# Performance work log

Hardware: AMD Instinct MI355X
Metric: run time of the kernel (lower is better)

The kernel has to match this reference:

```python
import jax, jax.numpy as jnp
import numpy as np

V = 50257  # vocab_size
H = 512    # d_model
S = 512    # source length
B = 8      # batch
T = 64     # decode steps


def setup_inputs() -> dict:
    key = jax.random.key(0)
    k1, k2, k3, k4, k5, k6 = jax.random.split(key, 6)
    src_full = jax.random.randint(k1, (S, B), 0, V, dtype=jnp.int32)
    decode_output = jax.random.normal(k2, (T, B, H), dtype=jnp.float32)
    decode_attn = jax.random.uniform(k3, (B, T, S), dtype=jnp.float32)
    memory = jax.random.normal(k4, (S, B, H), dtype=jnp.float32)
    # learned params: gen_proj (H->V) and prob_proj (H->1)
    W_gen = jax.random.normal(k5, (H, V), dtype=jnp.float32) / np.sqrt(H)
    b_gen = jnp.zeros((V,), dtype=jnp.float32)
    W_prob = jax.random.normal(k6, (H, 1), dtype=jnp.float32) / np.sqrt(H)
    b_prob = jnp.zeros((1,), dtype=jnp.float32)
    return {
        "src_full": src_full,
        "decode_output": decode_output,
        "decode_attn": decode_attn,
        "memory": memory,
        "W_gen": W_gen,
        "b_gen": b_gen,
        "W_prob": W_prob,
        "b_prob": b_prob,
    }


def reference(src_full, decode_output, decode_attn, memory, W_gen, b_gen, W_prob, b_prob):
    # context[t,b,h] = sum_s attn[b,t,s] * memory[s,b,h]
    context = jnp.einsum("bts,sbh->tbh", decode_attn, memory)  # [T,B,H]
    prob = jax.nn.sigmoid(context @ W_prob + b_prob)           # [T,B,1] copy gate p_gen
    gen_logits = prob * jax.nn.softmax(decode_output @ W_gen + b_gen, axis=-1)  # [T,B,V]

    # scatter-add attention mass onto vocab slots: copy[t,b, src_full[s,b]] += attn[b,t,s]
    attn_tbs = jnp.transpose(decode_attn, (1, 0, 2))  # [T,B,S]
    idx = src_full.T                                  # [B,S]
    ti = jnp.arange(T)[:, None, None]
    bi = jnp.arange(B)[None, :, None]
    copy_logits = jnp.zeros((T, B, V), dtype=decode_attn.dtype).at[ti, bi, idx[None, :, :]].add(attn_tbs)
    copy_logits = (1.0 - prob) * jax.nn.softmax(copy_logits, axis=-1)

    return jnp.log(gen_logits + copy_logits)
```

## Files before the change

kernel.cpp:

```cpp
#include <hip/hip_runtime.h>
#include <hip/hip_bf16.h>
#include <math.h>

#define VV 50257
#define VP 50304
#define HH 512
#define SS 512
#define BB 8
#define TT 64
#define MM (TT*BB)

typedef __bf16 bf16x2 __attribute__((ext_vector_type(2)));
typedef __bf16 bf16x4 __attribute__((ext_vector_type(4)));
typedef __bf16 bf16x8 __attribute__((ext_vector_type(8)));
typedef float  f32x4  __attribute__((ext_vector_type(4)));

__device__ __forceinline__ __bf16 f2b(float f) {
    unsigned u = __builtin_bit_cast(unsigned, f);
    unsigned r = (u + 0x7fffu + ((u >> 16) & 1u)) >> 16;
    unsigned short s = (unsigned short)r;
    return __builtin_bit_cast(__bf16, s);
}

__device__ __forceinline__ void gl2lds16(const void* g, void* l) {
    __builtin_amdgcn_global_load_lds(
        (const __attribute__((address_space(1))) unsigned*)g,
        (__attribute__((address_space(3))) unsigned*)l, 16, 0, 0);
}

#define WAITV(n) asm volatile("s_waitcnt vmcnt(" #n ")" ::: "memory")

__global__ __launch_bounds__(256) void k_pre0(const float* __restrict__ A,
                                              __bf16* __restrict__ Ab,
                                              const float* __restrict__ mem,
                                              const float* __restrict__ Wp,
                                              float* __restrict__ mw) {
    int tid = threadIdx.x;
    if (blockIdx.x < 256) {
        int i = (blockIdx.x * 256 + tid) * 4;
        float4 v = *(const float4*)&A[i];
        bf16x4 o = {f2b(v.x), f2b(v.y), f2b(v.z), f2b(v.w)};
        *(bf16x4*)&Ab[i] = o;
    } else {
        int bx = blockIdx.x - 256;
        int row = bx * 4 + (tid >> 6);
        int lane = tid & 63;
        const float* mp = mem + (size_t)row * HH;
        float acc = 0.f;
#pragma unroll
        for (int i = 0; i < HH / 64; i++)
            acc += mp[lane + 64 * i] * Wp[lane + 64 * i];
#pragma unroll
        for (int off = 32; off > 0; off >>= 1) acc += __shfl_down(acc, off);
        if (lane == 0) mw[row] = acc;
    }
}

#define NWT (VP / 32)
__global__ __launch_bounds__(256) void k_wt2(const float* __restrict__ W,
                                             __bf16* __restrict__ Wt,
                                             const float* __restrict__ attn,
                                             const float* __restrict__ mw,
                                             const float* __restrict__ bp,
                                             float* __restrict__ prob,
                                             float* __restrict__ Z) {
    __shared__ float tile[2][32][33];
    __shared__ __bf16 Wo[32][520];
    int tid = threadIdx.x;

    if (blockIdx.x < NWT) {
        int n0 = blockIdx.x * 32;
        int nn = tid >> 3, ks = (tid & 7) * 4;
#pragma unroll
        for (int kc = 0; kc < 16; kc++) {
            int k0 = kc * 32;
            int p = kc & 1;
#pragma unroll
            for (int rd = 0; rd < 4; rd++) {
                int idx = rd * 256 + tid;
                int kk = idx >> 5, nc = idx & 31;
                int n = n0 + nc;
                tile[p][kk][nc] = (n < VV) ? W[(size_t)(k0 + kk) * VV + n] : 0.f;
            }
            __syncthreads();
            bf16x4 o = {f2b(tile[p][ks][nn]), f2b(tile[p][ks + 1][nn]),
                        f2b(tile[p][ks + 2][nn]), f2b(tile[p][ks + 3][nn])};
            *(bf16x4*)&Wo[nn][k0 + ks] = o;
        }
        __syncthreads();
#pragma unroll
        for (int i = 0; i < 8; i++) {
            int r = i * 4 + (tid >> 6);
            int c = (tid & 63) * 8;
            *(bf16x8*)&Wt[(size_t)(n0 + r) * HH + c] = *(const bf16x8*)&Wo[r][c];
        }
    } else {
        int r = blockIdx.x - NWT;
        int t = r / BB, b = r % BB;
        const float* ap = attn + ((size_t)b * TT + t) * SS;
        float acc = ap[tid] * mw[tid * BB + b] +
                    ap[tid + 256] * mw[(tid + 256) * BB + b];
        float* red = &tile[0][0][0];
        red[tid] = acc; __syncthreads();
        for (int st = 128; st > 0; st >>= 1) {
            if (tid < st) red[tid] += red[tid + st];
            __syncthreads();
        }
        if (tid == 0) {
            prob[r] = 1.f / (1.f + expf(-(red[0] + bp[0])));
            Z[r] = 0.f;
        }
    }
}

template<bool BF16OUT>
__global__ __launch_bounds__(512, 4) void k_gemm6(const __bf16* __restrict__ Ab,
                                                  const __bf16* __restrict__ Wt,
                                                  const float* __restrict__ bias,
                                                  float* __restrict__ Cf,
                                                  __bf16* __restrict__ Cb,
                                                  float* __restrict__ Zrow) {
    __shared__ __bf16 As[3][8192];
    __shared__ __bf16 Bs[3][4096];
    __shared__ float zred[256];

    const int tid  = threadIdx.x;
    const int lane = tid & 63;
    const int wave = tid >> 6;
    const int l15  = lane & 15;
    const int quad = lane >> 4;
    const int wr = (wave >> 1) * 64;
    const int wc = (wave & 1) * 64;

    int L = blockIdx.x + gridDim.x * blockIdx.y;
    int xcd = L & 7, i8 = L >> 3;
    int nid = (xcd < 2 ? xcd * 99 : 2 * 99 + (xcd - 2) * 98) + i8;
    const int row0 = (nid & 1) * 256;
    const int col0 = (nid >> 1) * 128;

    size_t offA[2];
#pragma unroll
    for (int q = 0; q < 2; q++)
        offA[q] = (size_t)(row0 + (2 * wave + q) * 16 + l15) * HH + quad * 8;
    const size_t offB = (size_t)(col0 + wave * 16 + l15) * HH + quad * 8;

#define STAGE(buf, k0)                                                       \
    do {                                                                     \
        gl2lds16(Ab + offA[0] + (k0), &As[buf][(2 * wave) * 512]);           \
        gl2lds16(Ab + offA[1] + (k0), &As[buf][(2 * wave + 1) * 512]);       \
        gl2lds16(Wt + offB + (k0),    &Bs[buf][wave * 512]);                 \
    } while (0)

    f32x4 acc[4][4] = {};

    STAGE(0, 0);
    STAGE(1, 32);
#pragma unroll
    for (int it = 0; it < 16; ++it) {
        if (it < 15) WAITV(3);
        else         WAITV(0);
        __builtin_amdgcn_s_barrier();
        if (it < 14) STAGE((it + 2) % 3, (it + 2) * 32);
        const __bf16* Al = &As[it % 3][0];
        const __bf16* Bl = &Bs[it % 3][0];
        bf16x8 af[4], bfv[4];
#pragma unroll
        for (int mt = 0; mt < 4; mt++)
            af[mt] = *(const bf16x8*)&Al[((wr >> 4) + mt) * 512 + lane * 8];
#pragma unroll
        for (int nt = 0; nt < 4; nt++)
            bfv[nt] = *(const bf16x8*)&Bl[((wc >> 4) + nt) * 512 + lane * 8];
        __builtin_amdgcn_s_setprio(1);
#pragma unroll
        for (int mt = 0; mt < 4; mt++)
#pragma unroll
            for (int nt = 0; nt < 4; nt++)
                acc[mt][nt] = __builtin_amdgcn_mfma_f32_16x16x32_bf16(
                    af[mt], bfv[nt], acc[mt][nt], 0, 0, 0);
        __builtin_amdgcn_s_setprio(0);
    }
#undef STAGE

    __syncthreads();
    if (tid < 256) zred[tid] = 0.f;
    __syncthreads();

#pragma unroll
    for (int mt = 0; mt < 4; mt++) {
        float esum[4] = {0.f, 0.f, 0.f, 0.f};
#pragma unroll
        for (int nt = 0; nt < 4; nt++) {
            int c = col0 + wc + nt * 16 + l15;
            if (c < VV) {
                float bv = bias[c];
#pragma unroll
                for (int i = 0; i < 4; i++) {
                    int r = row0 + wr + mt * 16 + quad * 4 + i;
                    float l = acc[mt][nt][i] + bv;
                    if (BF16OUT) Cb[(size_t)r * VP + c] = f2b(l);
                    else         Cf[(size_t)r * VV + c] = l;
                    esum[i] += __expf(l);
                }
            }
        }
#pragma unroll
        for (int i = 0; i < 4; i++) {
            float e = esum[i];
            e += __shfl_xor(e, 1);
            e += __shfl_xor(e, 2);
            e += __shfl_xor(e, 4);
            e += __shfl_xor(e, 8);
            if (l15 == 0)
                atomicAdd(&zred[wr + mt * 16 + quad * 4 + i], e);
        }
    }
    __syncthreads();
    if (tid < 256) atomicAdd(&Zrow[row0 + tid], zred[tid]);
}

#define HT 1024
#define NBW 1572

__device__ __forceinline__ void build_hash(const int* __restrict__ src,
                                           const float* __restrict__ ap,
                                           int b, int tid,
                                           int* keys, float* vals, unsigned* bmap,
                                           float* red, int* s_D, float* s_Zc) {
    for (int i = tid; i < HT; i += 256) { keys[i] = -1; vals[i] = 0.f; }
    for (int i = tid; i < NBW; i += 256) bmap[i] = 0u;
    if (tid == 0) *s_D = 0;
    __syncthreads();

    for (int s = tid; s < SS; s += 256) {
        int idx = src[s * BB + b];
        float v = ap[s];
        unsigned h = ((unsigned)idx * 2654435761u) >> 22;
        while (true) {
            int old = atomicCAS(&keys[h], -1, idx);
            if (old == -1 || old == idx) { atomicAdd(&vals[h], v); break; }
            h = (h + 1) & (HT - 1);
        }
    }
    __syncthreads();

    float lsum = 0.f; int dloc = 0;
    for (int i = tid; i < HT; i += 256) {
        int k = keys[i];
        if (k != -1) {
            lsum += __expf(vals[i]); dloc++;
            atomicOr(&bmap[(unsigned)k >> 5], 1u << (k & 31));
        }
    }
    atomicAdd(s_D, dloc);
    red[tid] = lsum; __syncthreads();
    for (int st = 128; st > 0; st >>= 1) {
        if (tid < st) red[tid] += red[tid + st];
        __syncthreads();
    }
    if (tid == 0) *s_Zc = (float)(VV - *s_D) + red[0];
    __syncthreads();
}

#define HV (VP / 2)
__global__ __launch_bounds__(1024) void k_final2(const int* __restrict__ src,
                                                 const float* __restrict__ attn,
                                                 const float* __restrict__ prob,
                                                 const float* __restrict__ Zrow,
                                                 const __bf16* __restrict__ LG,
                                                 float* __restrict__ out) {
    __shared__ int      keys[HT];
    __shared__ float    vals[HT];
    __shared__ unsigned bmap[NBW];
    __shared__ float    red[1024];
    __shared__ int      s_D;
    __shared__ float    s_Zc;

    int r = blockIdx.y;
    int half = blockIdx.x;
    int t = r / BB, b = r % BB;
    int tid = threadIdx.x;
    const float* ap = attn + ((size_t)b * TT + t) * SS;

    { keys[tid] = -1; vals[tid] = 0.f; }
    for (int i = tid; i < NBW; i += 1024) bmap[i] = 0u;
    if (tid == 0) s_D = 0;
    __syncthreads();

    if (tid < SS) {
        int idx = src[tid * BB + b];
        float v = ap[tid];
        unsigned h = ((unsigned)idx * 2654435761u) >> 22;
        while (true) {
            int old = atomicCAS(&keys[h], -1, idx);
            if (old == -1 || old == idx) { atomicAdd(&vals[h], v); break; }
            h = (h + 1) & (HT - 1);
        }
    }
    __syncthreads();

    float lsum = 0.f;
    {
        int k = keys[tid];
        bool occ = (k != -1);
        if (occ) {
            lsum = __expf(vals[tid]);
            atomicOr(&bmap[(unsigned)k >> 5], 1u << (k & 31));
        }
        unsigned long long m = __ballot(occ);
        if ((tid & 63) == 0) atomicAdd(&s_D, __popcll(m));
    }
    red[tid] = lsum; __syncthreads();
    for (int st = 512; st > 0; st >>= 1) {
        if (tid < st) red[tid] += red[tid + st];
        __syncthreads();
    }
    if (tid == 0) s_Zc = (float)(VV - s_D) + red[0];
    __syncthreads();

    float p = prob[r];
    float pinvZ = p / Zrow[r];
    float qinvZc = (1.f - p) / s_Zc;

    const __bf16* lrow = LG + (size_t)r * VP;
    float* orow = out + (size_t)r * VV;

    int base = half * HV;
    for (int v0 = base + tid * 8; v0 < base + HV; v0 += 8192) {
        bf16x8 l8 = *(const bf16x8*)&lrow[v0];
        unsigned bits = (bmap[v0 >> 5] >> (v0 & 31)) & 0xFFu;
        if (bits == 0u && v0 + 8 <= VV) {
#pragma unroll
            for (int e = 0; e < 8; e++)
                orow[v0 + e] = __logf(pinvZ * __expf((float)l8[e]) + qinvZc);
        } else {
#pragma unroll
            for (int e = 0; e < 8; e++) {
                int v = v0 + e;
                if (v < VV) {
                    float l = (float)l8[e];
                    float c = 1.f;
                    if ((bits >> e) & 1u) {
                        unsigned h = ((unsigned)v * 2654435761u) >> 22;
                        while (true) {
                            int k = keys[h];
                            if (k == v) { c = __expf(vals[h]); break; }
                            if (k == -1) break;
                            h = (h + 1) & (HT - 1);
                        }
                    }
                    orow[v] = __logf(pinvZ * __expf(l) + qinvZc * c);
                }
            }
        }
    }
}

#define CHUNKS 6283
__global__ __launch_bounds__(256) void k_final_s(const int* __restrict__ src,
                                                 const float* __restrict__ attn,
                                                 const float* __restrict__ prob,
                                                 const float* __restrict__ Zrow,
                                                 float* __restrict__ out) {
    __shared__ int      keys[HT];
    __shared__ float    vals[HT];
    __shared__ unsigned bmap[NBW];
    __shared__ float    red[256];
    __shared__ int      s_D;
    __shared__ float    s_Zc;

    int r = blockIdx.y;
    int t = r / BB, b = r % BB;
    int tid = threadIdx.x;
    const float* ap = attn + ((size_t)b * TT + t) * SS;
    build_hash(src, ap, b, tid, keys, vals, bmap, red, &s_D, &s_Zc);

    float p = prob[r];
    float pinvZ = p / Zrow[r];
    float qinvZc = (1.f - p) / s_Zc;

    int c0 = blockIdx.x * CHUNKS;
    int c1 = c0 + CHUNKS; if (c1 > VV) c1 = VV;
    float* rowp = out + (size_t)r * VV;

    for (int v = c0 + tid; v < c1; v += 256) {
        float l = rowp[v];
        float c = 1.f;
        if ((bmap[v >> 5] >> (v & 31)) & 1u) {
            unsigned h = ((unsigned)v * 2654435761u) >> 22;
            while (true) {
                int k = keys[h];
                if (k == v) { c = __expf(vals[h]); break; }
                if (k == -1) break;
                h = (h + 1) & (HT - 1);
            }
        }
        rowp[v] = __logf(pinvZ * __expf(l) + qinvZc * c);
    }
}

extern "C" void kernel_launch(void* const* d_in, const int* in_sizes, int n_in,
                              void* d_out, int out_size, void* d_ws, size_t ws_size,
                              hipStream_t stream) {
    const int*   src_full      = (const int*)d_in[0];
    const float* decode_output = (const float*)d_in[1];
    const float* decode_attn   = (const float*)d_in[2];
    const float* memory        = (const float*)d_in[3];
    const float* W_gen         = (const float*)d_in[4];
    const float* b_gen         = (const float*)d_in[5];
    const float* W_prob        = (const float*)d_in[6];
    const float* b_prob        = (const float*)d_in[7];
    float* out = (float*)d_out;

    float* ws   = (float*)d_ws;
    float* mw   = ws;
    float* prob = ws + 4096;
    float* Z    = ws + 4608;
    __bf16* Ab  = (__bf16*)(ws + 5120);
    __bf16* Wt  = (__bf16*)(ws + 5120 + 131072);
    __bf16* LG  = Wt + (size_t)VP * HH;

    size_t base_b = (size_t)(5120 + 131072) * sizeof(float);
    size_t wt_b   = (size_t)VP * HH * 2;
    size_t lg_b   = (size_t)MM * VP * 2;
    bool full = ws_size >= base_b + wt_b + lg_b;

    k_pre0<<<1280, 256, 0, stream>>>(decode_output, Ab, memory, W_prob, mw);
    k_wt2<<<NWT + 512, 256, 0, stream>>>(W_gen, Wt, decode_attn, mw, b_prob,
                                         prob, Z);

    dim3 ggrid(MM / 256, VP / 128);
    if (full) {
        k_gemm6<true><<<ggrid, 512, 0, stream>>>(Ab, Wt, b_gen, nullptr, LG, Z);
        dim3 fgrid(2, MM);
        k_final2<<<fgrid, 1024, 0, stream>>>(src_full, decode_attn, prob, Z, LG, out);
    } else {
        k_gemm6<false><<<ggrid, 512, 0, stream>>>(Ab, Wt, b_gen, out, nullptr, Z);
        dim3 fgrid((VV + CHUNKS - 1) / CHUNKS, MM);
        k_final_s<<<fgrid, 256, 0, stream>>>(src_full, decode_attn, prob, Z, out);
    }
}
```

Before: 359.0 us.

## Use k-blocked W layout to drop LDS transpose and fold gate into final kernel

Replaces the LDS-tiled transpose of W_gen with a direct conversion into a k-blocked layout (8 consecutive k values per vocab column), written with vectorized loads and bf16x8 stores. The GEMM B-operand addressing is changed to read this layout. The conversion is merged into the pre-processing kernel, which removes one launch and the shared-memory round trip. The sigmoid copy gate is now computed inside the final kernels via an extra reduction, and Z is zeroed with a memset. The cost is redundant gate computation per final block and possibly less cache-friendly B loads in the GEMM.

```diff
diff --git a/kernel.cpp b/kernel.cpp
--- a/kernel.cpp
+++ b/kernel.cpp
@@ -14,6 +14,7 @@
 typedef __bf16 bf16x4 __attribute__((ext_vector_type(4)));
 typedef __bf16 bf16x8 __attribute__((ext_vector_type(8)));
 typedef float  f32x4  __attribute__((ext_vector_type(4)));
+typedef float f4u __attribute__((vector_size(16), aligned(4)));
 
 __device__ __forceinline__ __bf16 f2b(float f) {
     unsigned u = __builtin_bit_cast(unsigned, f);
@@ -30,20 +31,50 @@
 
 #define WAITV(n) asm volatile("s_waitcnt vmcnt(" #n ")" ::: "memory")
 
-__global__ __launch_bounds__(256) void k_pre0(const float* __restrict__ A,
-                                              __bf16* __restrict__ Ab,
-                                              const float* __restrict__ mem,
-                                              const float* __restrict__ Wp,
-                                              float* __restrict__ mw) {
+#define NW8 3200
+__global__ __launch_bounds__(256) void k_pre(const float* __restrict__ W,
+                                             __bf16* __restrict__ Wt8,
+                                             const float* __restrict__ A,
+                                             __bf16* __restrict__ Ab,
+                                             const float* __restrict__ mem,
+                                             const float* __restrict__ Wp,
+                                             float* __restrict__ mw) {
     int tid = threadIdx.x;
-    if (blockIdx.x < 256) {
-        int i = (blockIdx.x * 256 + tid) * 4;
-        float4 v = *(const float4*)&A[i];
-        bf16x4 o = {f2b(v.x), f2b(v.y), f2b(v.z), f2b(v.w)};
+    int bx = blockIdx.x;
+    if (bx < NW8) {
+        int cx = bx % 50, kb = bx / 50;
+        int nb = cx * 1024 + tid * 4;
+        if (nb >= VP) return;
+        const float* Wr = W + (size_t)(kb * 8) * VV + nb;
+        float v[8][4];
+        if (nb + 4 <= VV) {
+#pragma unroll
+            for (int r = 0; r < 8; r++) {
+                f4u x = *(const f4u*)(Wr + (size_t)r * VV);
+#pragma unroll
+                for (int j = 0; j < 4; j++) v[r][j] = x[j];
+            }
+        } else {
+#pragma unroll
+            for (int r = 0; r < 8; r++)
+#pragma unroll
+                for (int j = 0; j < 4; j++)
+                    v[r][j] = (nb + j < VV) ? Wr[(size_t)r * VV + j] : 0.f;
+        }
+#pragma unroll
+        for (int j = 0; j < 4; j++) {
+            bf16x8 o = {f2b(v[0][j]), f2b(v[1][j]), f2b(v[2][j]), f2b(v[3][j]),
+                        f2b(v[4][j]), f2b(v[5][j]), f2b(v[6][j]), f2b(v[7][j])};
+            *(bf16x8*)&Wt8[((size_t)kb * VP + nb + j) * 8] = o;
+        }
+    } else if (bx < NW8 + 256) {
+        int i = ((bx - NW8) * 256 + tid) * 4;
+        float4 va = *(const float4*)&A[i];
+        bf16x4 o = {f2b(va.x), f2b(va.y), f2b(va.z), f2b(va.w)};
         *(bf16x4*)&Ab[i] = o;
     } else {
-        int bx = blockIdx.x - 256;
-        int row = bx * 4 + (tid >> 6);
+        int bxm = bx - (NW8 + 256);
+        int row = bxm * 4 + (tid >> 6);
         int lane = tid & 63;
         const float* mp = mem + (size_t)row * HH;
         float acc = 0.f;
@@ -56,66 +87,9 @@
     }
 }
 
-#define NWT (VP / 32)
-__global__ __launch_bounds__(256) void k_wt2(const float* __restrict__ W,
-                                             __bf16* __restrict__ Wt,
-                                             const float* __restrict__ attn,
-                                             const float* __restrict__ mw,
-                                             const float* __restrict__ bp,
-                                             float* __restrict__ prob,
-                                             float* __restrict__ Z) {
-    __shared__ float tile[2][32][33];
-    __shared__ __bf16 Wo[32][520];
-    int tid = threadIdx.x;
-
-    if (blockIdx.x < NWT) {
-        int n0 = blockIdx.x * 32;
-        int nn = tid >> 3, ks = (tid & 7) * 4;
-#pragma unroll
-        for (int kc = 0; kc < 16; kc++) {
-            int k0 = kc * 32;
-            int p = kc & 1;
-#pragma unroll
-            for (int rd = 0; rd < 4; rd++) {
-                int idx = rd * 256 + tid;
-                int kk = idx >> 5, nc = idx & 31;
-                int n = n0 + nc;
-                tile[p][kk][nc] = (n < VV) ? W[(size_t)(k0 + kk) * VV + n] : 0.f;
-            }
-            __syncthreads();
-            bf16x4 o = {f2b(tile[p][ks][nn]), f2b(tile[p][ks + 1][nn]),
-                        f2b(tile[p][ks + 2][nn]), f2b(tile[p][ks + 3][nn])};
-            *(bf16x4*)&Wo[nn][k0 + ks] = o;
-        }
-        __syncthreads();
-#pragma unroll
-        for (int i = 0; i < 8; i++) {
-            int r = i * 4 + (tid >> 6);
-            int c = (tid & 63) * 8;
-            *(bf16x8*)&Wt[(size_t)(n0 + r) * HH + c] = *(const bf16x8*)&Wo[r][c];
-        }
-    } else {
-        int r = blockIdx.x - NWT;
-        int t = r / BB, b = r % BB;
-        const float* ap = attn + ((size_t)b * TT + t) * SS;
-        float acc = ap[tid] * mw[tid * BB + b] +
-                    ap[tid + 256] * mw[(tid + 256) * BB + b];
-        float* red = &tile[0][0][0];
-        red[tid] = acc; __syncthreads();
-        for (int st = 128; st > 0; st >>= 1) {
-            if (tid < st) red[tid] += red[tid + st];
-            __syncthreads();
-        }
-        if (tid == 0) {
-            prob[r] = 1.f / (1.f + expf(-(red[0] + bp[0])));
-            Z[r] = 0.f;
-        }
-    }
-}
-
 template<bool BF16OUT>
-__global__ __launch_bounds__(512, 4) void k_gemm6(const __bf16* __restrict__ Ab,
-                                                  const __bf16* __restrict__ Wt,
+__global__ __launch_bounds__(512, 4) void k_gemm7(const __bf16* __restrict__ Ab,
+                                                  const __bf16* __restrict__ Wt8,
                                                   const float* __restrict__ bias,
                                                   float* __restrict__ Cf,
                                                   __bf16* __restrict__ Cb,
@@ -142,13 +116,14 @@
 #pragma unroll
     for (int q = 0; q < 2; q++)
         offA[q] = (size_t)(row0 + (2 * wave + q) * 16 + l15) * HH + quad * 8;
-    const size_t offB = (size_t)(col0 + wave * 16 + l15) * HH + quad * 8;
+    const size_t offB = (size_t)quad * VP * 8 +
+                        (size_t)(col0 + wave * 16 + l15) * 8;
 
 #define STAGE(buf, k0)                                                       \
     do {                                                                     \
         gl2lds16(Ab + offA[0] + (k0), &As[buf][(2 * wave) * 512]);           \
         gl2lds16(Ab + offA[1] + (k0), &As[buf][(2 * wave + 1) * 512]);       \
-        gl2lds16(Wt + offB + (k0),    &Bs[buf][wave * 512]);                 \
+        gl2lds16(Wt8 + offB + (size_t)(k0) * VP, &Bs[buf][wave * 512]);      \
     } while (0)
 
     f32x4 acc[4][4] = {};
@@ -264,7 +239,8 @@
 #define HV (VP / 2)
 __global__ __launch_bounds__(1024) void k_final2(const int* __restrict__ src,
                                                  const float* __restrict__ attn,
-                                                 const float* __restrict__ prob,
+                                                 const float* __restrict__ mw,
+                                                 const float* __restrict__ bp,
                                                  const float* __restrict__ Zrow,
                                                  const __bf16* __restrict__ LG,
                                                  float* __restrict__ out) {
@@ -272,8 +248,10 @@
     __shared__ float    vals[HT];
     __shared__ unsigned bmap[NBW];
     __shared__ float    red[1024];
+    __shared__ float    red2[1024];
     __shared__ int      s_D;
     __shared__ float    s_Zc;
+    __shared__ float    s_p;
 
     int r = blockIdx.y;
     int half = blockIdx.x;
@@ -286,13 +264,15 @@
     if (tid == 0) s_D = 0;
     __syncthreads();
 
+    float pv = 0.f;
     if (tid < SS) {
         int idx = src[tid * BB + b];
-        float v = ap[tid];
+        float av = ap[tid];
+        pv = av * mw[tid * BB + b];
         unsigned h = ((unsigned)idx * 2654435761u) >> 22;
         while (true) {
             int old = atomicCAS(&keys[h], -1, idx);
-            if (old == -1 || old == idx) { atomicAdd(&vals[h], v); break; }
+            if (old == -1 || old == idx) { atomicAdd(&vals[h], av); break; }
             h = (h + 1) & (HT - 1);
         }
     }
@@ -309,15 +289,18 @@
         unsigned long long m = __ballot(occ);
         if ((tid & 63) == 0) atomicAdd(&s_D, __popcll(m));
     }
-    red[tid] = lsum; __syncthreads();
+    red[tid] = lsum; red2[tid] = pv; __syncthreads();
     for (int st = 512; st > 0; st >>= 1) {
-        if (tid < st) red[tid] += red[tid + st];
+        if (tid < st) { red[tid] += red[tid + st]; red2[tid] += red2[tid + st]; }
         __syncthreads();
     }
-    if (tid == 0) s_Zc = (float)(VV - s_D) + red[0];
-    __syncthreads();
-
-    float p = prob[r];
+    if (tid == 0) {
+        s_Zc = (float)(VV - s_D) + red[0];
+        s_p  = 1.f / (1.f + expf(-(red2[0] + bp[0])));
+    }
+    __syncthreads();
+
+    float p = s_p;
     float pinvZ = p / Zrow[r];
     float qinvZc = (1.f - p) / s_Zc;
 
@@ -358,7 +341,8 @@
 #define CHUNKS 6283
 __global__ __launch_bounds__(256) void k_final_s(const int* __restrict__ src,
                                                  const float* __restrict__ attn,
-                                                 const float* __restrict__ prob,
+                                                 const float* __restrict__ mw,
+                                                 const float* __restrict__ bp,
                                                  const float* __restrict__ Zrow,
                                                  float* __restrict__ out) {
     __shared__ int      keys[HT];
@@ -367,14 +351,26 @@
     __shared__ float    red[256];
     __shared__ int      s_D;
     __shared__ float    s_Zc;
+    __shared__ float    s_p;
 
     int r = blockIdx.y;
     int t = r / BB, b = r % BB;
     int tid = threadIdx.x;
     const float* ap = attn + ((size_t)b * TT + t) * SS;
+
+    float pacc = ap[tid] * mw[tid * BB + b] +
+                 ap[tid + 256] * mw[(tid + 256) * BB + b];
+    red[tid] = pacc; __syncthreads();
+    for (int st = 128; st > 0; st >>= 1) {
+        if (tid < st) red[tid] += red[tid + st];
+        __syncthreads();
+    }
+    if (tid == 0) s_p = 1.f / (1.f + expf(-(red[0] + bp[0])));
+    __syncthreads();
+
     build_hash(src, ap, b, tid, keys, vals, bmap, red, &s_D, &s_Zc);
 
-    float p = prob[r];
+    float p = s_p;
     float pinvZ = p / Zrow[r];
     float qinvZc = (1.f - p) / s_Zc;
 
@@ -413,29 +409,30 @@
 
     float* ws   = (float*)d_ws;
     float* mw   = ws;
-    float* prob = ws + 4096;
     float* Z    = ws + 4608;
     __bf16* Ab  = (__bf16*)(ws + 5120);
-    __bf16* Wt  = (__bf16*)(ws + 5120 + 131072);
-    __bf16* LG  = Wt + (size_t)VP * HH;
+    __bf16* Wt8 = (__bf16*)(ws + 5120 + 131072);
+    __bf16* LG  = Wt8 + (size_t)VP * HH;
 
     size_t base_b = (size_t)(5120 + 131072) * sizeof(float);
     size_t wt_b   = (size_t)VP * HH * 2;
     size_t lg_b   = (size_t)MM * VP * 2;
     bool full = ws_size >= base_b + wt_b + lg_b;
 
-    k_pre0<<<1280, 256, 0, stream>>>(decode_output, Ab, memory, W_prob, mw);
-    k_wt2<<<NWT + 512, 256, 0, stream>>>(W_gen, Wt, decode_attn, mw, b_prob,
-                                         prob, Z);
+    k_pre<<<NW8 + 256 + 1024, 256, 0, stream>>>(
+        W_gen, Wt8, decode_output, Ab, memory, W_prob, mw);
+    hipMemsetAsync(Z, 0, MM * sizeof(float), stream);
 
     dim3 ggrid(MM / 256, VP / 128);
     if (full) {
-        k_gemm6<true><<<ggrid, 512, 0, stream>>>(Ab, Wt, b_gen, nullptr, LG, Z);
+        k_gemm7<true><<<ggrid, 512, 0, stream>>>(Ab, Wt8, b_gen, nullptr, LG, Z);
         dim3 fgrid(2, MM);
-        k_final2<<<fgrid, 1024, 0, stream>>>(src_full, decode_attn, prob, Z, LG, out);
+        k_final2<<<fgrid, 1024, 0, stream>>>(src_full, decode_attn, mw, b_prob,
+                                             Z, LG, out);
     } else {
-        k_gemm6<false><<<ggrid, 512, 0, stream>>>(Ab, Wt, b_gen, out, nullptr, Z);
+        k_gemm7<false><<<ggrid, 512, 0, stream>>>(Ab, Wt8, b_gen, out, nullptr, Z);
         dim3 fgrid((VV + CHUNKS - 1) / CHUNKS, MM);
-        k_final_s<<<fgrid, 256, 0, stream>>>(src_full, decode_attn, prob, Z, out);
-    }
-}
+        k_final_s<<<fgrid, 256, 0, stream>>>(src_full, decode_attn, mw, b_prob,
+                                             Z, out);
+    }
+}
```

Measured after the change: 311.5 us. -13.2%, faster.
